# Optimization experiments

Hardware: AMD Instinct MI355X
Metric: run time of the kernel (lower is better)

## Reference

```python
import jax, jax.numpy as jnp
import numpy as np

N_NODES = 50000
N_EDGES = 400000
IN_DIM = 128
HIDDEN = 128
OUT_DIM = 128
MIX = 4

def _gelu(x):
    return jax.nn.gelu(x, approximate=False)  # torch default erf-GELU

def setup_inputs() -> dict:
    key = jax.random.key(0)
    ks = jax.random.split(key, 8)
    X = jax.random.normal(ks[0], (N_NODES, IN_DIM), dtype=jnp.float32)
    edge_index = jax.random.randint(ks[1], (2, N_EDGES), 0, N_NODES, dtype=jnp.int64)
    s = lambda fan_in: 1.0 / np.sqrt(fan_in)
    W1 = jax.random.uniform(ks[2], (HIDDEN, IN_DIM), jnp.float32, -s(IN_DIM), s(IN_DIM))
    b1 = jax.random.uniform(ks[3], (HIDDEN,), jnp.float32, -s(IN_DIM), s(IN_DIM))
    WA = jax.random.uniform(ks[4], (HIDDEN, HIDDEN), jnp.float32, -s(HIDDEN), s(HIDDEN))
    WB = jax.random.uniform(ks[5], (MIX, HIDDEN), jnp.float32, -s(HIDDEN), s(HIDDEN))
    W2 = jax.random.uniform(ks[6], (OUT_DIM, 2 * HIDDEN), jnp.float32, -s(2 * HIDDEN), s(2 * HIDDEN))
    b2 = jax.random.uniform(ks[7], (OUT_DIM,), jnp.float32, -s(2 * HIDDEN), s(2 * HIDDEN))
    return {"X": X, "edge_index": edge_index, "W1": W1, "b1": b1,
            "WA": WA, "WB": WB, "W2": W2, "b2": b2}

def reference(X, edge_index, W1, b1, WA, WB, W2, b2):
    num_nodes = X.shape[0]
    # ff1 -> gelu (dropout identity in eval)
    H = _gelu(X @ W1.T + b1)                       # (N, h)
    src, dst = edge_index[0], edge_index[1]
    X_src = H[src]                                 # (E, h) gather
    # hyper target weights per edge
    W_tar = _gelu(X_src @ WA.T) @ WB.T             # (E, m)
    # per-edge outer product, scatter_add over dst
    cross = X_src[:, :, None] * W_tar[:, None, :]  # (E, h, m)
    agg = jax.ops.segment_sum(cross, dst, num_segments=num_nodes)  # (N, h, m)
    agg = _gelu(agg)
    # gather back per edge, contract mix dim
    out_edge = jnp.einsum('ehm,em->eh', agg[dst], W_tar)  # (E, h)
    # scatter_mean over dst
    ones = jnp.ones((src.shape[0],), X.dtype)
    cnt = jax.ops.segment_sum(ones, dst, num_segments=num_nodes)   # (N,)
    agg_node = jax.ops.segment_sum(out_edge, dst, num_segments=num_nodes)
    agg_node = agg_node / jnp.maximum(cnt, 1.0)[:, None]           # (N, h)
    # root connection + gelu, ff2
    feat = _gelu(jnp.concatenate([agg_node, H], axis=1))           # (N, 2h)
    out = feat @ W2.T + b2                                          # (N, out)
    return out
```

## Files before the change

### kernel.cpp

```cpp
#include <hip/hip_runtime.h>
#include <hip/hip_bf16.h>

#define NN 50000
#define NE 400000
#define NT 3125

typedef unsigned short u16;
typedef short short8 __attribute__((ext_vector_type(8)));
typedef float f32x4 __attribute__((ext_vector_type(4)));

__device__ __forceinline__ float geluf(float x){ return 0.5f*x*(1.0f+erff(x*0.70710678118654752440f)); }
__device__ __forceinline__ u16 f2bfb(float f){
  union { __hip_bfloat16 h; u16 u; } cv; cv.h = __float2bfloat16(f); return cv.u;
}
__device__ __forceinline__ float bfb2f(u16 u){ return __uint_as_float(((unsigned)u)<<16); }

__global__ __launch_bounds__(256) void k_zero(int4* __restrict__ p){
  int i = blockIdx.x*256 + threadIdx.x;
  if (i < 25024) p[i] = (int4){0,0,0,0};
}

__global__ __launch_bounds__(256) void k_pre(const float* __restrict__ W1,
    const float* __restrict__ WA, const float* __restrict__ W2,
    u16* __restrict__ W1b, u16* __restrict__ WAb, u16* __restrict__ W2r,
    const int* __restrict__ dst, int* __restrict__ deg)
{
  if (blockIdx.x < 32){
    int i4 = (blockIdx.x*256 + threadIdx.x) * 4;
    const float* srcp; u16* dstp; int off;
    if (i4 < 16384){ srcp = W1; dstp = W1b; off = i4; }
    else { srcp = WA; dstp = WAb; off = i4 - 16384; }
    float4 v = *(const float4*)(srcp + off);
    ushort4 o;
    o.x = f2bfb(v.x); o.y = f2bfb(v.y); o.z = f2bfb(v.z); o.w = f2bfb(v.w);
    *(ushort4*)(dstp + off) = o;
  } else if (blockIdx.x < 48){
    int t0 = (blockIdx.x - 32)*2048 + threadIdx.x*8;
    int lane = (t0 >> 3) & 63;
    int kk   = (t0 >> 9) & 7;
    int nb   = t0 >> 12;
    int src  = (nb*16 + (lane & 15))*256 + kk*32 + (lane >> 4)*8;
    float4 v0 = *(const float4*)(W2 + src);
    float4 v1 = *(const float4*)(W2 + src + 4);
    ushort4 o0, o1;
    o0.x = f2bfb(v0.x); o0.y = f2bfb(v0.y); o0.z = f2bfb(v0.z); o0.w = f2bfb(v0.w);
    o1.x = f2bfb(v1.x); o1.y = f2bfb(v1.y); o1.z = f2bfb(v1.z); o1.w = f2bfb(v1.w);
    *(ushort4*)(W2r + t0)     = o0;
    *(ushort4*)(W2r + t0 + 4) = o1;
  } else {
    int e = (blockIdx.x - 48)*256 + threadIdx.x;
    if (e < NE) atomicAdd(&deg[dst[e]], 1);
  }
}

__global__ __launch_bounds__(512) void k_ff1n(const float* __restrict__ X,
    const u16* __restrict__ W1b, const float* __restrict__ b1,
    const u16* __restrict__ WAb, const float* __restrict__ WB,
    u16* __restrict__ Hb, float* __restrict__ T)
{
  extern __shared__ u16 smem[];
  u16* w1s = smem;
  u16* was = smem + 17408;
  const int LDW = 136;
  for (int idx8 = threadIdx.x*8; idx8 < 128*128; idx8 += 512*8){
    int c = idx8 >> 7, k = idx8 & 127;
    *(short8*)&w1s[c*LDW + k] = *(const short8*)(W1b + idx8);
    *(short8*)&was[c*LDW + k] = *(const short8*)(WAb + idx8);
  }
  __syncthreads();
  const int lane = threadIdx.x & 63;
  const int wave = threadIdx.x >> 6;
  const int lrow = lane & 15;
  const int kgrp = lane >> 4;
  u16* hls = smem + 34816 + wave*(16*LDW);
  float4 b1v[8];
  #pragma unroll
  for (int nb = 0; nb < 8; nb++) b1v[nb] = *(const float4*)(b1 + nb*16 + kgrp*4);
  float wbv[4][8];
  #pragma unroll
  for (int m = 0; m < 4; m++)
    #pragma unroll
    for (int nb = 0; nb < 8; nb++)
      wbv[m][nb] = WB[m*128 + nb*16 + lrow];
  for (int tile = blockIdx.x*8 + wave; tile < NT; tile += gridDim.x*8){
    const float* xr = X + (size_t)(tile*16 + lrow)*128 + kgrp*8;
    f32x4 acc[8];
    #pragma unroll
    for (int nb = 0; nb < 8; nb++) acc[nb] = (f32x4){0.f,0.f,0.f,0.f};
    #pragma unroll
    for (int kk = 0; kk < 4; kk++){
      float4 xa = *(const float4*)(xr + kk*32);
      float4 xb = *(const float4*)(xr + kk*32 + 4);
      union { short8 v; u16 u[8]; } af;
      af.u[0]=f2bfb(xa.x); af.u[1]=f2bfb(xa.y); af.u[2]=f2bfb(xa.z); af.u[3]=f2bfb(xa.w);
      af.u[4]=f2bfb(xb.x); af.u[5]=f2bfb(xb.y); af.u[6]=f2bfb(xb.z); af.u[7]=f2bfb(xb.w);
      #pragma unroll
      for (int nb = 0; nb < 8; nb++){
        short8 bf = *(const short8*)&w1s[(nb*16 + lrow)*LDW + kk*32 + kgrp*8];
        acc[nb] = __builtin_amdgcn_mfma_f32_16x16x32_bf16(bf, af.v, acc[nb], 0, 0, 0);
      }
    }
    const size_t rb = (size_t)(tile*16 + lrow)*128 + kgrp*4;
    #pragma unroll
    for (int nb = 0; nb < 8; nb++){
      ushort4 hp;
      #pragma unroll
      for (int r = 0; r < 4; r++)
        ((u16*)&hp)[r] = f2bfb(geluf(acc[nb][r] + b1v[nb][r]));
      *(ushort4*)(Hb + rb + nb*16) = hp;
      *(ushort4*)&hls[lrow*LDW + nb*16 + kgrp*4] = hp;
    }
    f32x4 acc2[8];
    #pragma unroll
    for (int nb = 0; nb < 8; nb++) acc2[nb] = (f32x4){0.f,0.f,0.f,0.f};
    #pragma unroll
    for (int kk = 0; kk < 4; kk++){
      short8 af = *(const short8*)&hls[lrow*LDW + kk*32 + kgrp*8];
      #pragma unroll
      for (int nb = 0; nb < 8; nb++){
        short8 bf = *(const short8*)&was[(nb*16 + lrow)*LDW + kk*32 + kgrp*8];
        acc2[nb] = __builtin_amdgcn_mfma_f32_16x16x32_bf16(af, bf, acc2[nb], 0, 0, 0);
      }
    }
    float part[4][4];
    #pragma unroll
    for (int r = 0; r < 4; r++)
      #pragma unroll
      for (int m = 0; m < 4; m++) part[r][m] = 0.f;
    #pragma unroll
    for (int nb = 0; nb < 8; nb++){
      float g0 = geluf(acc2[nb][0]), g1 = geluf(acc2[nb][1]);
      float g2 = geluf(acc2[nb][2]), g3 = geluf(acc2[nb][3]);
      #pragma unroll
      for (int m = 0; m < 4; m++){
        float w = wbv[m][nb];
        part[0][m] += g0*w; part[1][m] += g1*w;
        part[2][m] += g2*w; part[3][m] += g3*w;
      }
    }
    #pragma unroll
    for (int s = 1; s < 16; s <<= 1)
      #pragma unroll
      for (int r = 0; r < 4; r++)
        #pragma unroll
        for (int m = 0; m < 4; m++)
          part[r][m] += __shfl_xor(part[r][m], s, 64);
    if (lrow == 0){
      #pragma unroll
      for (int r = 0; r < 4; r++){
        f32x4 tv = { part[r][0], part[r][1], part[r][2], part[r][3] };
        *(f32x4*)&T[(size_t)(tile*16 + kgrp*4 + r)*4] = tv;
      }
    }
  }
}

__global__ __launch_bounds__(1024) void k_scan(const int* __restrict__ deg, int* __restrict__ offs){
  __shared__ int wsum[16];
  __shared__ int sbase_s;
  const int tid = threadIdx.x, lane = tid & 63, wave = tid >> 6;
  if (tid == 0) sbase_s = 0;
  __syncthreads();
  for (int base = 0; base < NN; base += 4096){
    int i0 = base + tid*4;
    int v0=0,v1=0,v2=0,v3=0;
    if (i0+3 < NN){ int4 v = *(const int4*)(deg+i0); v0=v.x;v1=v.y;v2=v.z;v3=v.w; }
    else {
      if (i0   < NN) v0 = deg[i0];
      if (i0+1 < NN) v1 = deg[i0+1];
      if (i0+2 < NN) v2 = deg[i0+2];
    }
    int own = v0+v1+v2+v3;
    int inc = own;
    #pragma unroll
    for (int s=1;s<64;s<<=1){ int t = __shfl_up(inc, s, 64); if (lane >= s) inc += t; }
    if (lane == 63) wsum[wave] = inc;
    __syncthreads();
    if (wave == 0 && lane < 16){
      int w = wsum[lane];
      #pragma unroll
      for (int s=1;s<16;s<<=1){ int t = __shfl_up(w, s, 64); if (lane >= s) w += t; }
      wsum[lane] = w;
    }
    __syncthreads();
    int sbase = sbase_s;
    int wbase = sbase + (wave ? wsum[wave-1] : 0);
    int excl = wbase + inc - own;
    if (i0   < NN) offs[i0]   = excl;
    if (i0+1 < NN) offs[i0+1] = excl + v0;
    if (i0+2 < NN) offs[i0+2] = excl + v0+v1;
    if (i0+3 < NN) offs[i0+3] = excl + v0+v1+v2;
    __syncthreads();
    if (tid == 0) sbase_s = sbase + wsum[15];
    __syncthreads();
  }
  if (tid == 0) offs[NN] = sbase_s;
}

__global__ void k_fill(const int* __restrict__ src, const int* __restrict__ dst,
                       const int* __restrict__ offs, int* __restrict__ cur,
                       int* __restrict__ slist){
  int e = blockIdx.x*256 + threadIdx.x;
  if (e < NE){
    int d = dst[e];
    int p = atomicAdd(&cur[d], 1);
    slist[offs[d] + p] = src[e];
  }
}

__global__ __launch_bounds__(256) void k_agg(const u16* __restrict__ Hb,
    const float* __restrict__ T, const int* __restrict__ offs,
    const int* __restrict__ slist, u16* __restrict__ GAb)
{
  const int lane = threadIdx.x & 63;
  const int wave = threadIdx.x >> 6;
  const int vo = lane*2;
  for (int v = blockIdx.x*4 + wave; v < NN; v += gridDim.x*4){
    const int e0 = __builtin_amdgcn_readfirstlane(offs[v]);
    const int e1 = __builtin_amdgcn_readfirstlane(offs[v+1]);
    float ax0=0, ax1=0, ax2=0, ax3=0;
    float ay0=0, ay1=0, ay2=0, ay3=0;
    float s0=0, s1=0, s2=0, s3=0;
    int idx = e0;
    for (; idx + 8 <= e1; idx += 8){
      unsigned pk[8]; float4 tt[8];
      #pragma unroll
      for (int u = 0; u < 8; u++){
        int sn = slist[idx+u];
        pk[u] = *(const unsigned*)(Hb + (size_t)sn*128 + vo);
        tt[u] = *(const float4*)(T + (size_t)sn*4);
      }
      #pragma unroll
      for (int u = 0; u < 8; u++){
        float hx = bfb2f((u16)(pk[u] & 0xffffu));
        float hy = bfb2f((u16)(pk[u] >> 16));
        ax0 += hx*tt[u].x; ax1 += hx*tt[u].y; ax2 += hx*tt[u].z; ax3 += hx*tt[u].w;
        ay0 += hy*tt[u].x; ay1 += hy*tt[u].y; ay2 += hy*tt[u].z; ay3 += hy*tt[u].w;
        s0 += tt[u].x; s1 += tt[u].y; s2 += tt[u].z; s3 += tt[u].w;
      }
    }
    for (; idx + 4 <= e1; idx += 4){
      unsigned pk[4]; float4 tt[4];
      #pragma unroll
      for (int u = 0; u < 4; u++){
        int sn = slist[idx+u];
        pk[u] = *(const unsigned*)(Hb + (size_t)sn*128 + vo);
        tt[u] = *(const float4*)(T + (size_t)sn*4);
      }
      #pragma unroll
      for (int u = 0; u < 4; u++){
        float hx = bfb2f((u16)(pk[u] & 0xffffu));
        float hy = bfb2f((u16)(pk[u] >> 16));
        ax0 += hx*tt[u].x; ax1 += hx*tt[u].y; ax2 += hx*tt[u].z; ax3 += hx*tt[u].w;
        ay0 += hy*tt[u].x; ay1 += hy*tt[u].y; ay2 += hy*tt[u].z; ay3 += hy*tt[u].w;
        s0 += tt[u].x; s1 += tt[u].y; s2 += tt[u].z; s3 += tt[u].w;
      }
    }
    for (; idx < e1; idx++){
      int sn = slist[idx];
      unsigned pk = *(const unsigned*)(Hb + (size_t)sn*128 + vo);
      float hx = bfb2f((u16)(pk & 0xffffu));
      float hy = bfb2f((u16)(pk >> 16));
      float4 wt = *(const float4*)(T + (size_t)sn*4);
      ax0 += hx*wt.x; ax1 += hx*wt.y; ax2 += hx*wt.z; ax3 += hx*wt.w;
      ay0 += hy*wt.x; ay1 += hy*wt.y; ay2 += hy*wt.z; ay3 += hy*wt.w;
      s0 += wt.x; s1 += wt.y; s2 += wt.z; s3 += wt.w;
    }
    float inv = 1.0f / fmaxf((float)(e1 - e0), 1.0f);
    float ox = geluf(ax0)*s0 + geluf(ax1)*s1 + geluf(ax2)*s2 + geluf(ax3)*s3;
    float oy = geluf(ay0)*s0 + geluf(ay1)*s1 + geluf(ay2)*s2 + geluf(ay3)*s3;
    ushort2 res;
    res.x = f2bfb(geluf(ox * inv));
    res.y = f2bfb(geluf(oy * inv));
    *(ushort2*)(GAb + (size_t)v*128 + vo) = res;
  }
}

__global__ __launch_bounds__(256, 4) void k_ff2(const u16* __restrict__ GAb,
    const u16* __restrict__ Hb, const u16* __restrict__ W2r,
    const float* __restrict__ b2, float* __restrict__ out)
{
  const int lane = threadIdx.x & 63;
  const int wave = threadIdx.x >> 6;
  const int lrow = lane & 15;
  const int kgrp = lane >> 4;
  const int widx = blockIdx.x*4 + wave;
  const int tile = widx >> 1;
  const int nbh  = (widx & 1)*4;
  if (tile >= NT) return;
  const int row = tile*16 + lrow;
  short8 a[8];
  {
    const u16* ga = GAb + (size_t)row*128 + kgrp*8;
    const u16* hb = Hb  + (size_t)row*128 + kgrp*8;
    #pragma unroll
    for (int kk = 0; kk < 4; kk++){
      a[kk]   = *(const short8*)(ga + kk*32);
      a[4+kk] = *(const short8*)(hb + kk*32);
    }
    #pragma unroll
    for (int kk = 4; kk < 8; kk++){
      union { short8 v; u16 u[8]; } g;
      #pragma unroll
      for (int j = 0; j < 8; j++)
        g.u[j] = f2bfb(geluf(bfb2f(((const u16*)&a[kk])[j])));
      a[kk] = g.v;
    }
  }
  f32x4 acc[4];
  #pragma unroll
  for (int q = 0; q < 4; q++) acc[q] = (f32x4){0.f,0.f,0.f,0.f};
  const u16* wbase = W2r + lane*8;
  #pragma unroll
  for (int kk = 0; kk < 8; kk++){
    #pragma unroll
    for (int q = 0; q < 4; q++){
      short8 bf = *(const short8*)(wbase + (size_t)((nbh + q)*8 + kk)*512);
      acc[q] = __builtin_amdgcn_mfma_f32_16x16x32_bf16(bf, a[kk], acc[q], 0, 0, 0);
    }
  }
  float* orp = out + (size_t)row*128 + nbh*16 + kgrp*4;
  #pragma unroll
  for (int q = 0; q < 4; q++){
    float4 bv = *(const float4*)(b2 + (nbh + q)*16 + kgrp*4);
    f32x4 o;
    o[0] = acc[q][0] + bv.x;
    o[1] = acc[q][1] + bv.y;
    o[2] = acc[q][2] + bv.z;
    o[3] = acc[q][3] + bv.w;
    *(f32x4*)(orp + q*16) = o;
  }
}

extern "C" void kernel_launch(void* const* d_in, const int* in_sizes, int n_in,
                              void* d_out, int out_size, void* d_ws, size_t ws_size,
                              hipStream_t stream)
{
  (void)in_sizes; (void)n_in; (void)out_size; (void)ws_size;
  const float* X  = (const float*)d_in[0];
  const int*   ei = (const int*)d_in[1];
  const float* W1 = (const float*)d_in[2];
  const float* b1 = (const float*)d_in[3];
  const float* WA = (const float*)d_in[4];
  const float* WB = (const float*)d_in[5];
  const float* W2 = (const float*)d_in[6];
  const float* b2 = (const float*)d_in[7];
  float* out = (float*)d_out;
  const int* src = ei;
  const int* dst = ei + NE;

  char* p = (char*)d_ws;
  u16*   Hb   = (u16*)(p);
  u16*   GAb  = (u16*)(p + 12800000);
  float* T    = (float*)(p + 25600000);
  int*   deg  = (int*)(p + 26400000);
  int*   cur  = (int*)(p + 26600192);
  int*   offs = (int*)(p + 26800384);
  int*   slist= (int*)(p + 27000832);
  u16*   W1b  = (u16*)(p + 28600832);
  u16*   WAb  = (u16*)(p + 28633600);
  u16*   W2r  = (u16*)(p + 28666368);

  (void)hipFuncSetAttribute((const void*)k_ff1n, hipFuncAttributeMaxDynamicSharedMemorySize, 104448);

  k_zero<<<98, 256, 0, stream>>>((int4*)deg);
  k_pre <<<48 + (NE+255)/256, 256, 0, stream>>>(W1, WA, W2, W1b, WAb, W2r, dst, deg);
  k_ff1n<<<391, 512, 104448, stream>>>(X, W1b, b1, WAb, WB, Hb, T);
  k_scan<<<1, 1024, 0, stream>>>(deg, offs);
  k_fill<<<(NE+255)/256, 256, 0, stream>>>(src, dst, offs, cur, slist);
  k_agg <<<2048, 256, 0, stream>>>(Hb, T, offs, slist, GAb);
  k_ff2 <<<(2*NT+3)/4, 256, 0, stream>>>(GAb, Hb, W2r, b2, out);
}
```

Before: 144.4 us.

## Fuse aggregation and ff2 GEMM into one kernel via shared-memory tile

Merges the per-node aggregation kernel with the final ff2 MFMA GEMM. Each block computes 16 nodes' aggregated features, stages them in LDS, then each wave computes 32 output columns for the tile. This removes the GAb round-trip through global memory and one kernel launch. In exchange, blocks are now fixed to 16 nodes with no grid-stride loop, the 4-wide remainder loop is dropped, and the aggregation and GEMM phases run serially within each block.

```diff
diff --git a/kernel.cpp b/kernel.cpp
--- a/kernel.cpp
+++ b/kernel.cpp
@@ -208,14 +208,23 @@
   }
 }
 
-__global__ __launch_bounds__(256) void k_agg(const u16* __restrict__ Hb,
+__global__ __launch_bounds__(256) void k_aggff2(const u16* __restrict__ Hb,
     const float* __restrict__ T, const int* __restrict__ offs,
-    const int* __restrict__ slist, u16* __restrict__ GAb)
+    const int* __restrict__ slist, const u16* __restrict__ W2r,
+    const float* __restrict__ b2, float* __restrict__ out)
 {
+  __shared__ u16 gls[16*136];
+  const int LDW = 136;
   const int lane = threadIdx.x & 63;
   const int wave = threadIdx.x >> 6;
+  const int lrow = lane & 15;
+  const int kgrp = lane >> 4;
+  const int tile = blockIdx.x;
   const int vo = lane*2;
-  for (int v = blockIdx.x*4 + wave; v < NN; v += gridDim.x*4){
+
+  #pragma unroll
+  for (int r = 0; r < 4; r++){
+    const int v = tile*16 + wave*4 + r;
     const int e0 = __builtin_amdgcn_readfirstlane(offs[v]);
     const int e1 = __builtin_amdgcn_readfirstlane(offs[v+1]);
     float ax0=0, ax1=0, ax2=0, ax3=0;
@@ -232,23 +241,6 @@
       }
       #pragma unroll
       for (int u = 0; u < 8; u++){
-        float hx = bfb2f((u16)(pk[u] & 0xffffu));
-        float hy = bfb2f((u16)(pk[u] >> 16));
-        ax0 += hx*tt[u].x; ax1 += hx*tt[u].y; ax2 += hx*tt[u].z; ax3 += hx*tt[u].w;
-        ay0 += hy*tt[u].x; ay1 += hy*tt[u].y; ay2 += hy*tt[u].z; ay3 += hy*tt[u].w;
-        s0 += tt[u].x; s1 += tt[u].y; s2 += tt[u].z; s3 += tt[u].w;
-      }
-    }
-    for (; idx + 4 <= e1; idx += 4){
-      unsigned pk[4]; float4 tt[4];
-      #pragma unroll
-      for (int u = 0; u < 4; u++){
-        int sn = slist[idx+u];
-        pk[u] = *(const unsigned*)(Hb + (size_t)sn*128 + vo);
-        tt[u] = *(const float4*)(T + (size_t)sn*4);
-      }
-      #pragma unroll
-      for (int u = 0; u < 4; u++){
         float hx = bfb2f((u16)(pk[u] & 0xffffu));
         float hy = bfb2f((u16)(pk[u] >> 16));
         ax0 += hx*tt[u].x; ax1 += hx*tt[u].y; ax2 += hx*tt[u].z; ax3 += hx*tt[u].w;
@@ -272,32 +264,20 @@
     ushort2 res;
     res.x = f2bfb(geluf(ox * inv));
     res.y = f2bfb(geluf(oy * inv));
-    *(ushort2*)(GAb + (size_t)v*128 + vo) = res;
-  }
-}
-
-__global__ __launch_bounds__(256, 4) void k_ff2(const u16* __restrict__ GAb,
-    const u16* __restrict__ Hb, const u16* __restrict__ W2r,
-    const float* __restrict__ b2, float* __restrict__ out)
-{
-  const int lane = threadIdx.x & 63;
-  const int wave = threadIdx.x >> 6;
-  const int lrow = lane & 15;
-  const int kgrp = lane >> 4;
-  const int widx = blockIdx.x*4 + wave;
-  const int tile = widx >> 1;
-  const int nbh  = (widx & 1)*4;
-  if (tile >= NT) return;
+    *(ushort2*)&gls[(wave*4 + r)*LDW + vo] = res;
+  }
+  __syncthreads();
+
   const int row = tile*16 + lrow;
   short8 a[8];
+  #pragma unroll
+  for (int kk = 0; kk < 4; kk++)
+    a[kk] = *(const short8*)&gls[lrow*LDW + kk*32 + kgrp*8];
   {
-    const u16* ga = GAb + (size_t)row*128 + kgrp*8;
-    const u16* hb = Hb  + (size_t)row*128 + kgrp*8;
-    #pragma unroll
-    for (int kk = 0; kk < 4; kk++){
-      a[kk]   = *(const short8*)(ga + kk*32);
+    const u16* hb = Hb + (size_t)row*128 + kgrp*8;
+    #pragma unroll
+    for (int kk = 0; kk < 4; kk++)
       a[4+kk] = *(const short8*)(hb + kk*32);
-    }
     #pragma unroll
     for (int kk = 4; kk < 8; kk++){
       union { short8 v; u16 u[8]; } g;
@@ -307,22 +287,22 @@
       a[kk] = g.v;
     }
   }
-  f32x4 acc[4];
-  #pragma unroll
-  for (int q = 0; q < 4; q++) acc[q] = (f32x4){0.f,0.f,0.f,0.f};
+  f32x4 acc[2];
+  acc[0] = (f32x4){0.f,0.f,0.f,0.f};
+  acc[1] = (f32x4){0.f,0.f,0.f,0.f};
   const u16* wbase = W2r + lane*8;
   #pragma unroll
   for (int kk = 0; kk < 8; kk++){
     #pragma unroll
-    for (int q = 0; q < 4; q++){
-      short8 bf = *(const short8*)(wbase + (size_t)((nbh + q)*8 + kk)*512);
+    for (int q = 0; q < 2; q++){
+      short8 bf = *(const short8*)(wbase + (size_t)((wave*2 + q)*8 + kk)*512);
       acc[q] = __builtin_amdgcn_mfma_f32_16x16x32_bf16(bf, a[kk], acc[q], 0, 0, 0);
     }
   }
-  float* orp = out + (size_t)row*128 + nbh*16 + kgrp*4;
-  #pragma unroll
-  for (int q = 0; q < 4; q++){
-    float4 bv = *(const float4*)(b2 + (nbh + q)*16 + kgrp*4);
+  float* orp = out + (size_t)row*128 + wave*32 + kgrp*4;
+  #pragma unroll
+  for (int q = 0; q < 2; q++){
+    float4 bv = *(const float4*)(b2 + (wave*2 + q)*16 + kgrp*4);
     f32x4 o;
     o[0] = acc[q][0] + bv.x;
     o[1] = acc[q][1] + bv.y;
@@ -351,23 +331,21 @@
 
   char* p = (char*)d_ws;
   u16*   Hb   = (u16*)(p);
-  u16*   GAb  = (u16*)(p + 12800000);
-  float* T    = (float*)(p + 25600000);
-  int*   deg  = (int*)(p + 26400000);
-  int*   cur  = (int*)(p + 26600192);
-  int*   offs = (int*)(p + 26800384);
-  int*   slist= (int*)(p + 27000832);
-  u16*   W1b  = (u16*)(p + 28600832);
-  u16*   WAb  = (u16*)(p + 28633600);
-  u16*   W2r  = (u16*)(p + 28666368);
+  float* T    = (float*)(p + 12800000);
+  int*   deg  = (int*)(p + 13600000);
+  int*   cur  = (int*)(p + 13800192);
+  int*   offs = (int*)(p + 14000384);
+  int*   slist= (int*)(p + 14200832);
+  u16*   W1b  = (u16*)(p + 15800832);
+  u16*   WAb  = (u16*)(p + 15833600);
+  u16*   W2r  = (u16*)(p + 15866368);
 
   (void)hipFuncSetAttribute((const void*)k_ff1n, hipFuncAttributeMaxDynamicSharedMemorySize, 104448);
 
-  k_zero<<<98, 256, 0, stream>>>((int4*)deg);
-  k_pre <<<48 + (NE+255)/256, 256, 0, stream>>>(W1, WA, W2, W1b, WAb, W2r, dst, deg);
-  k_ff1n<<<391, 512, 104448, stream>>>(X, W1b, b1, WAb, WB, Hb, T);
-  k_scan<<<1, 1024, 0, stream>>>(deg, offs);
-  k_fill<<<(NE+255)/256, 256, 0, stream>>>(src, dst, offs, cur, slist);
-  k_agg <<<2048, 256, 0, stream>>>(Hb, T, offs, slist, GAb);
-  k_ff2 <<<(2*NT+3)/4, 256, 0, stream>>>(GAb, Hb, W2r, b2, out);
-}
+  k_zero  <<<98, 256, 0, stream>>>((int4*)deg);
+  k_pre   <<<48 + (NE+255)/256, 256, 0, stream>>>(W1, WA, W2, W1b, WAb, W2r, dst, deg);
+  k_ff1n  <<<391, 512, 104448, stream>>>(X, W1b, b1, WAb, WB, Hb, T);
+  k_scan  <<<1, 1024, 0, stream>>>(deg, offs);
+  k_fill  <<<(NE+255)/256, 256, 0, stream>>>(src, dst, offs, cur, slist);
+  k_aggff2<<<NT, 256, 0, stream>>>(Hb, T, offs, slist, W2r, b2, out);
+}
```

Result: slower. 167.0 us (+15.6%).
